# Performance work log

Measured on AMD Instinct MI355X. Metric: run time of the kernel, lower is better.

## Reference

```python
import jax, jax.numpy as jnp
import numpy as np
from jax import lax

RES = 3072
L = 20000

def setup_inputs() -> dict:
    key = jax.random.key(0)
    k1, k2, k3 = jax.random.split(key, 3)
    data = jax.random.uniform(k1, (L, 1), dtype=jnp.float32)
    Win = jax.random.uniform(k2, (RES, 2), dtype=jnp.float32) - 0.5
    W = jax.random.uniform(k3, (RES, RES), dtype=jnp.float32) - 0.5
    # spectral radius of iid uniform(-0.5,0.5) NxN is ~ sqrt(N/12); rescale to 1.25
    W = W * (1.25 / np.sqrt(RES / 12.0)).astype(np.float32)
    return {"data": data, "Win": Win, "W": W,
            "trainLen": 4000, "testLen": 16000, "initLen": 100, "errorLen": 500}

def reference(data, Win, W, trainLen, testLen, initLen, errorLen):
    a = jnp.float32(0.3)
    reg = jnp.float32(4.84e-07)
    res_size = W.shape[0]
    dt = data.dtype

    def train_step(x, u):  # x: [res], u: [1]
        inp = jnp.concatenate([jnp.ones((1,), dt), u])        # [2]
        x = (1 - a) * x + a * jnp.tanh(Win @ inp + W @ x)
        return x, x

    x0 = jnp.zeros((res_size,), dt)
    x_last, xs = lax.scan(train_step, x0, data[:trainLen])     # xs: [trainLen, res]

    n = trainLen - initLen
    # X: rows = [1; u_t; x_t], columns t = initLen..trainLen-1  -> [2+res, n]
    Xmat = jnp.concatenate([jnp.ones((n, 1), dt), data[initLen:trainLen], xs[initLen:]], axis=1).T
    Yt = data[initLen + 1:trainLen + 1]                        # [n, 1]
    A = Xmat @ Xmat.T + reg * jnp.eye(res_size + 2, dtype=dt)
    B = Xmat @ Yt                                              # [2+res, 1]
    Wout = jnp.linalg.solve(A, B).T                            # [1, 2+res]

    def test_step(carry, _):
        x, u = carry
        inp = jnp.concatenate([jnp.ones((1,), dt), u])
        x = (1 - a) * x + a * jnp.tanh(Win @ inp + W @ x)
        out = jnp.concatenate([jnp.ones((1,), dt), u, x])      # [2+res]
        y = Wout @ out                                         # [1]
        return (x, y), y

    u0 = data[trainLen]
    _, Y = lax.scan(test_step, (x_last, u0), None, length=testLen)
    return Y  # [testLen, 1]
```

## Files before the change

kernel.cpp:

```cpp
#include <hip/hip_runtime.h>
#include <math.h>

#define NWG 256
#define TPB 256
#define NWGR 128
#define TPBR 512

constexpr int RES   = 3072;
constexpr int NCOL  = 3074;
constexpr int LDA_  = 3136;
constexpr int TRAIN = 4000;
constexpr int INITN = 100;
constexpr int TESTN = 16000;
constexpr int NSAMP = TRAIN - INITN;
constexpr int NB    = (NCOL + 63) / 64;
constexpr float REGC = 4.84e-07f;

constexpr size_t OFF_PKT_TR  = 4096;
constexpr size_t OFF_ROOT_TR = 8192;
constexpr size_t OFF_PKT_TE  = 12288;
constexpr size_t OFF_ROOT_TE = 16384;
constexpr size_t OFF_F1      = 20480;
constexpr size_t OFF_F2      = 24576;
constexpr size_t OFF_WOUT    = 28672;
constexpr size_t OFF_X       = 49152;
constexpr size_t OFF_B       = 81920;
constexpr size_t OFF_WV      = 114688;
constexpr size_t OFF_Z       = 262144;
constexpr size_t OFF_A       = 50331648;

typedef unsigned long long u64;

#define ALOAD_U32(p)     __hip_atomic_load((p), __ATOMIC_RELAXED, __HIP_MEMORY_SCOPE_AGENT)
#define ALOAD_U64(p)     __hip_atomic_load((p), __ATOMIC_RELAXED, __HIP_MEMORY_SCOPE_AGENT)
#define ASTORE_U64(p, v) __hip_atomic_store((p), (v), __ATOMIC_RELAXED, __HIP_MEMORY_SCOPE_AGENT)
#define AADD_U64(p, v)   __hip_atomic_fetch_add((p), (v), __ATOMIC_RELAXED, __HIP_MEMORY_SCOPE_AGENT)

__device__ __forceinline__ u64 pack_partial(float pf) {
    pf = fminf(fmaxf(pf, -1e6f), 1e6f);
    long long ll = (long long)(pf * 65536.0f);
    return ((u64)ll << 16) + 1ULL;
}

__device__ __forceinline__ u64 hbar(u64* pkt1, u64* root, int s, int g, int tid, u64 arrival) {
    const int ph = s % 3;
    const int grp = g >> 3;
    __builtin_amdgcn_s_waitcnt(0);
    __syncthreads();
    __shared__ u64 rres;
    if (tid == 0) {
        AADD_U64(&pkt1[(ph * 16 + grp) * 8], arrival);
        if ((g & 7) == 0) {
            u64 p;
            do { p = ALOAD_U64(&pkt1[(ph * 16 + grp) * 8]); } while ((p & 0xFFFFULL) != 8ULL);
            AADD_U64(&root[ph * 8], (p & ~0xFFFFULL) | 1ULL);
        }
        u64 r;
        for (;;) {
            r = ALOAD_U64(&root[ph * 8]);
            if ((r & 0xFFFFULL) == 16ULL) break;
            __builtin_amdgcn_s_sleep(1);
        }
        rres = r;
        const int ph2 = (s + 2) % 3;
        if ((g & 7) == 0) ASTORE_U64(&pkt1[(ph2 * 16 + grp) * 8], 0ULL);
        if (g == 0) ASTORE_U64(&root[ph2 * 8], 0ULL);
    }
    __syncthreads();
    return rres;
}

__device__ __forceinline__ void fbar(unsigned* flags, unsigned ep) {
    __threadfence();
    __syncthreads();
    if (threadIdx.x == 0)
        __hip_atomic_store(&flags[blockIdx.x], ep, __ATOMIC_RELEASE, __HIP_MEMORY_SCOPE_AGENT);
    for (;;) {
        unsigned f = ALOAD_U32(&flags[threadIdx.x]);
        if (__syncthreads_and((int)(f >= ep))) break;
        __builtin_amdgcn_s_sleep(1);
    }
    __threadfence();
}

__global__ void k_init(char* __restrict__ ws) {
    size_t tid = (size_t)blockIdx.x * blockDim.x + threadIdx.x;
    size_t nthr = (size_t)gridDim.x * blockDim.x;
    float4 z4 = make_float4(0.f, 0.f, 0.f, 0.f);
    float4* p0 = (float4*)ws;
    for (size_t i = tid; i < 131072 / 16; i += nthr) p0[i] = z4;
    float4* pz = (float4*)(ws + OFF_Z);
    size_t nz = (size_t)NSAMP * LDA_ / 4;
    for (size_t i = tid; i < nz; i += nthr) pz[i] = z4;
}

__global__ __launch_bounds__(512, 2) void k_train(const float* __restrict__ data,
                                                  const float* __restrict__ Win,
                                                  const float* __restrict__ W,
                                                  char* __restrict__ ws) {
    __shared__ float xs[RES];
    float* xb = (float*)(ws + OFF_X);
    float* Z  = (float*)(ws + OFF_Z);
    u64* pkt1 = (u64*)(ws + OFF_PKT_TR);
    u64* root = (u64*)(ws + OFF_ROOT_TR);
    const int tid = threadIdx.x, g = blockIdx.x;
    const int w = tid >> 6, l = tid & 63;
    const int row0 = g * 24 + w * 3;
    const int myrow = row0 + l;
    const float4* W4 = (const float4*)W;
    float4 wreg[36];
#pragma unroll
    for (int r = 0; r < 3; r++)
#pragma unroll
        for (int j = 0; j < 12; j++)
            wreg[r * 12 + j] = W4[(size_t)(row0 + r) * 768 + l + 64 * j];
    float wi0 = 0.f, wi1 = 0.f;
    if (l < 3) { wi0 = Win[2 * myrow]; wi1 = Win[2 * myrow + 1]; }
    const float a_ = 0.3f, oma = 1.0f - 0.3f;
#pragma unroll 1
    for (int s = 0; s < TRAIN; s++) {
        u64* xc8 = (u64*)(xb + (s & 1) * RES);
        float* xn = xb + ((s + 1) & 1) * RES;
        float u = data[s];
        u64* xs8 = (u64*)xs;
#pragma unroll
        for (int p = 0; p < 3; p++)
            xs8[tid + p * TPBR] = ALOAD_U64(&xc8[tid + p * TPBR]);
        __syncthreads();
        float acc0 = 0.f, acc1 = 0.f, acc2 = 0.f;
#pragma unroll
        for (int j = 0; j < 12; j++) {
            float4 xv = ((const float4*)xs)[l + 64 * j];
            float4 w0 = wreg[j], w1 = wreg[12 + j], w2 = wreg[24 + j];
            acc0 += w0.x * xv.x + w0.y * xv.y + w0.z * xv.z + w0.w * xv.w;
            acc1 += w1.x * xv.x + w1.y * xv.y + w1.z * xv.z + w1.w * xv.w;
            acc2 += w2.x * xv.x + w2.y * xv.y + w2.z * xv.z + w2.w * xv.w;
        }
#pragma unroll
        for (int off = 32; off; off >>= 1) {
            acc0 += __shfl_xor(acc0, off);
            acc1 += __shfl_xor(acc1, off);
            acc2 += __shfl_xor(acc2, off);
        }
        if (l < 3) {
            float acc = (l == 0) ? acc0 : ((l == 1) ? acc1 : acc2);
            float pre = acc + wi0 + wi1 * u;
            float xo = xs[myrow];
            float xv_ = oma * xo + a_ * tanhf(pre);
            __hip_atomic_store(&xn[myrow], xv_, __ATOMIC_RELAXED, __HIP_MEMORY_SCOPE_AGENT);
            if (s >= INITN) Z[(size_t)(s - INITN) * LDA_ + 2 + myrow] = xv_;
        }
        if (g == 0 && tid == 0 && s >= INITN) {
            Z[(size_t)(s - INITN) * LDA_] = 1.0f;
            Z[(size_t)(s - INITN) * LDA_ + 1] = u;
        }
        hbar(pkt1, root, s, g, tid, 1ULL);
    }
}

__global__ __launch_bounds__(256) void k_syrk(char* __restrict__ ws) {
    __shared__ float As[64 * 64];
    __shared__ float Bs[64 * 64];
    double* A = (double*)(ws + OFF_A);
    const float4* Z4 = (const float4*)(ws + OFF_Z);
    int tt = blockIdx.x, tid = threadIdx.x;
    int bi = 0;
    while ((bi + 1) * (bi + 2) / 2 <= tt) bi++;
    int bj = tt - bi * (bi + 1) / 2;
    double a64[4][4];
#pragma unroll
    for (int i = 0; i < 4; i++)
#pragma unroll
        for (int j = 0; j < 4; j++) a64[i][j] = 0.0;
    int di = tid & 15, dj = tid >> 4;
    for (int t0 = 0; t0 < NSAMP; t0 += 64) {
#pragma unroll
        for (int p = 0; p < 4; p++) {
            int idx = tid + p * 256;
            int tl = idx >> 4, q = idx & 15;
            float4 va = make_float4(0.f, 0.f, 0.f, 0.f), vb = va;
            if (t0 + tl < NSAMP) {
                va = Z4[(size_t)(t0 + tl) * 784 + bi * 16 + q];
                vb = Z4[(size_t)(t0 + tl) * 784 + bj * 16 + q];
            }
            *(float4*)&As[tl * 64 + q * 4] = va;
            *(float4*)&Bs[tl * 64 + q * 4] = vb;
        }
        __syncthreads();
#pragma unroll 4
        for (int kk = 0; kk < 64; kk++) {
            float4 av = *(const float4*)&As[kk * 64 + di * 4];
            float4 bv = *(const float4*)&Bs[kk * 64 + dj * 4];
            double ad[4] = {(double)av.x, (double)av.y, (double)av.z, (double)av.w};
            double bd[4] = {(double)bv.x, (double)bv.y, (double)bv.z, (double)bv.w};
#pragma unroll
            for (int ii = 0; ii < 4; ii++)
#pragma unroll
                for (int jj = 0; jj < 4; jj++) a64[ii][jj] += ad[ii] * bd[jj];
        }
        __syncthreads();
    }
#pragma unroll
    for (int ii = 0; ii < 4; ii++) {
        int gi = bi * 64 + di * 4 + ii;
#pragma unroll
        for (int jj = 0; jj < 4; jj++) {
            int gj = bj * 64 + dj * 4 + jj;
            if (gi < NCOL && gj < NCOL) {
                double v = a64[ii][jj];
                if (gi == gj) v += (double)REGC;
                A[(size_t)gi * LDA_ + gj] = v;
            }
        }
    }
}

__global__ void k_bvec(const float* __restrict__ data, char* __restrict__ ws) {
    const float* Z = (const float*)(ws + OFF_Z);
    double* b = (double*)(ws + OFF_B);
    int gi = blockIdx.x * blockDim.x + threadIdx.x;
    if (gi >= NCOL) return;
    double acc0 = 0, acc1 = 0, acc2 = 0, acc3 = 0;
    int t = 0;
    for (; t + 3 < NSAMP; t += 4) {
        acc0 += (double)Z[(size_t)t * LDA_ + gi] * (double)data[INITN + t + 1];
        acc1 += (double)Z[(size_t)(t + 1) * LDA_ + gi] * (double)data[INITN + t + 2];
        acc2 += (double)Z[(size_t)(t + 2) * LDA_ + gi] * (double)data[INITN + t + 3];
        acc3 += (double)Z[(size_t)(t + 3) * LDA_ + gi] * (double)data[INITN + t + 4];
    }
    for (; t < NSAMP; t++) acc0 += (double)Z[(size_t)t * LDA_ + gi] * (double)data[INITN + t + 1];
    b[gi] = (acc0 + acc1) + (acc2 + acc3);
}

__global__ __launch_bounds__(256, 1) void k_chol(char* __restrict__ ws) {
    __shared__ double sm[8192];
    double* A = (double*)(ws + OFF_A);
    unsigned* flags = (unsigned*)(ws + OFF_F1);
    unsigned ep = 0;
    int tid = threadIdx.x;
#pragma unroll 1
    for (int k = 0; k < NB; k++) {
        int K = k * 64;
        int bs = NCOL - K; if (bs > 64) bs = 64;
        if (blockIdx.x == 0) {
            for (int idx = tid; idx < bs * bs; idx += TPB) {
                int i = idx / bs, j = idx - i * bs;
                sm[i * 64 + j] = A[(size_t)(K + i) * LDA_ + K + j];
            }
            __syncthreads();
#pragma unroll 1
            for (int j = 0; j < bs; j++) {
                if (tid == 0) {
                    double dv = sm[j * 64 + j];
                    sm[j * 64 + j] = (dv > 0.0) ? sqrt(dv) : 1e-150;
                }
                __syncthreads();
                double d = sm[j * 64 + j];
                for (int i = j + 1 + tid; i < bs; i += TPB) sm[i * 64 + j] /= d;
                __syncthreads();
                int i = tid & 63, mw = tid >> 6;
                if (i > j && i < bs) {
                    double lij = sm[i * 64 + j];
                    for (int m = j + 1 + mw; m <= i; m += 4) sm[i * 64 + m] -= lij * sm[m * 64 + j];
                }
                __syncthreads();
            }
            for (int idx = tid; idx < bs * bs; idx += TPB) {
                int i = idx / bs, j = idx - i * bs;
                if (j <= i) A[(size_t)(K + i) * LDA_ + K + j] = sm[i * 64 + j];
            }
        }
        fbar(flags, ++ep);
        if (K + 64 < NCOL) {
            for (int idx = tid; idx < 4096; idx += TPB) {
                int i = idx >> 6, j = idx & 63;
                sm[i * 64 + j] = A[(size_t)(K + i) * LDA_ + K + j];
            }
            __syncthreads();
            int row = K + 64 + blockIdx.x * TPB + tid;
            if (row < NCOL) {
                double r[64];
#pragma unroll
                for (int j = 0; j < 64; j++) r[j] = A[(size_t)row * LDA_ + K + j];
#pragma unroll
                for (int j = 0; j < 64; j++) {
                    double s = r[j];
#pragma unroll
                    for (int m = 0; m < j; m++) s -= r[m] * sm[j * 64 + m];
                    r[j] = s / sm[j * 64 + j];
                }
#pragma unroll
                for (int j = 0; j < 64; j++) A[(size_t)row * LDA_ + K + j] = r[j];
            }
            fbar(flags, ++ep);
            int rem = NCOL - (K + 64);
            int nbt = (rem + 63) / 64;
            int ntt = nbt * nbt + nbt;
            double* LikT = sm;
            double* LjkT = sm + 4160;
            int i0 = (tid & 15) * 4, j0 = (tid >> 4) * 2;
#pragma unroll 1
            for (int tt = blockIdx.x; tt < ntt; tt += NWG) {
                int ti = 0;
                while ((ti + 1) * (ti + 2) <= tt) ti++;
                int tj = tt - ti * (ti + 1);
                int I0 = K + 64 + ti * 64, J0 = K + 64 + tj * 32;
                for (int idx = tid; idx < 4096; idx += TPB) {
                    int kk = idx & 63, ii = idx >> 6;
                    double v = (I0 + ii < NCOL) ? A[(size_t)(I0 + ii) * LDA_ + K + kk] : 0.0;
                    LikT[kk * 65 + ii] = v;
                }
                for (int idx = tid; idx < 2048; idx += TPB) {
                    int kk = idx & 63, jj = idx >> 6;
                    double v = (J0 + jj < NCOL) ? A[(size_t)(J0 + jj) * LDA_ + K + kk] : 0.0;
                    LjkT[kk * 33 + jj] = v;
                }
                __syncthreads();
                double c[4][2];
#pragma unroll
                for (int ii = 0; ii < 4; ii++)
#pragma unroll
                    for (int jj = 0; jj < 2; jj++) {
                        int gi = I0 + i0 + ii, gj = J0 + j0 + jj;
                        c[ii][jj] = (gi < NCOL && gj < NCOL) ? A[(size_t)gi * LDA_ + gj] : 0.0;
                    }
#pragma unroll 4
                for (int kk = 0; kk < 64; kk++) {
                    double a0 = LikT[kk * 65 + i0], a1 = LikT[kk * 65 + i0 + 1];
                    double a2 = LikT[kk * 65 + i0 + 2], a3 = LikT[kk * 65 + i0 + 3];
                    double b0 = LjkT[kk * 33 + j0], b1 = LjkT[kk * 33 + j0 + 1];
                    c[0][0] -= a0 * b0; c[0][1] -= a0 * b1;
                    c[1][0] -= a1 * b0; c[1][1] -= a1 * b1;
                    c[2][0] -= a2 * b0; c[2][1] -= a2 * b1;
                    c[3][0] -= a3 * b0; c[3][1] -= a3 * b1;
                }
#pragma unroll
                for (int ii = 0; ii < 4; ii++)
#pragma unroll
                    for (int jj = 0; jj < 2; jj++) {
                        int gi = I0 + i0 + ii, gj = J0 + j0 + jj;
                        if (gi < NCOL && gj < NCOL) A[(size_t)gi * LDA_ + gj] = c[ii][jj];
                    }
                __syncthreads();
            }
            fbar(flags, ++ep);
        }
    }
}

__global__ __launch_bounds__(256, 1) void k_solve(char* __restrict__ ws) {
    __shared__ double smd[4096];
    __shared__ double wl[64];
    double* A = (double*)(ws + OFF_A);
    double* b = (double*)(ws + OFF_B);
    double* wv = (double*)(ws + OFF_WV);
    float* wout = (float*)(ws + OFF_WOUT);
    unsigned* flags = (unsigned*)(ws + OFF_F2);
    unsigned ep = 0;
    int tid = threadIdx.x;
#pragma unroll 1
    for (int kb = 0; kb < NB; kb++) {
        int K = kb * 64, bs = NCOL - K; if (bs > 64) bs = 64;
        if (blockIdx.x == 0) {
            for (int idx = tid; idx < 4096; idx += TPB) {
                int i = idx >> 6, j = idx & 63;
                smd[idx] = (i < bs && j < bs) ? A[(size_t)(K + i) * LDA_ + K + j] : ((i == j) ? 1.0 : 0.0);
            }
            __syncthreads();
            if (tid < 64) {
                double bl = (tid < bs) ? b[K + tid] : 0.0;
                for (int j = 0; j < bs; j++) {
                    if (tid == j) bl /= smd[j * 64 + j];
                    double bj = __shfl(bl, j, 64);
                    if (tid > j) bl -= smd[tid * 64 + j] * bj;
                }
                if (tid < bs) b[K + tid] = bl;
            }
        }
        fbar(flags, ++ep);
        if (K + 64 < NCOL) {
            if (tid < 64) wl[tid] = b[K + tid];
            __syncthreads();
            int i = K + 64 + blockIdx.x * TPB + tid;
            if (i < NCOL) {
                double s = 0.0;
#pragma unroll 8
                for (int m = 0; m < 64; m++) s += A[(size_t)i * LDA_ + K + m] * wl[m];
                b[i] -= s;
            }
        }
        fbar(flags, ++ep);
    }
#pragma unroll 1
    for (int kb = NB - 1; kb >= 0; kb--) {
        int K = kb * 64, bs = NCOL - K; if (bs > 64) bs = 64;
        if (blockIdx.x == 0) {
            for (int idx = tid; idx < 4096; idx += TPB) {
                int i = idx >> 6, j = idx & 63;
                smd[idx] = (i < bs && j < bs) ? A[(size_t)(K + i) * LDA_ + K + j] : ((i == j) ? 1.0 : 0.0);
            }
            __syncthreads();
            if (tid < 64) {
                double bl = (tid < bs) ? b[K + tid] : 0.0;
                for (int j = bs - 1; j >= 0; j--) {
                    if (tid == j) bl /= smd[j * 64 + j];
                    double wj = __shfl(bl, j, 64);
                    if (tid < j) bl -= smd[j * 64 + tid] * wj;
                }
                if (tid < bs) wv[K + tid] = bl;
            }
        }
        fbar(flags, ++ep);
        if (K > 0) {
            if (tid < 64) wl[tid] = (tid < bs) ? wv[K + tid] : 0.0;
            __syncthreads();
            int i = blockIdx.x * TPB + tid;
            if (i < K) {
                double s = 0.0;
                for (int m = 0; m < bs; m++) s += A[(size_t)(K + m) * LDA_ + i] * wl[m];
                b[i] -= s;
            }
        }
        fbar(flags, ++ep);
    }
    int gi = blockIdx.x * TPB + tid;
    if (gi < NCOL) wout[gi] = (float)wv[gi];
}

__global__ __launch_bounds__(512, 2) void k_test(const float* __restrict__ data,
                                                 const float* __restrict__ Win,
                                                 const float* __restrict__ W,
                                                 char* __restrict__ ws,
                                                 float* __restrict__ out) {
    __shared__ float xs[RES];
    __shared__ float wp[8];
    float* xb = (float*)(ws + OFF_X);
    const float* wout = (const float*)(ws + OFF_WOUT);
    u64* pkt1 = (u64*)(ws + OFF_PKT_TE);
    u64* root = (u64*)(ws + OFF_ROOT_TE);
    const int tid = threadIdx.x, g = blockIdx.x;
    const int w = tid >> 6, l = tid & 63;
    const int row0 = g * 24 + w * 3;
    const int myrow = row0 + l;
    const float4* W4 = (const float4*)W;
    float4 wreg[36];
#pragma unroll
    for (int r = 0; r < 3; r++)
#pragma unroll
        for (int j = 0; j < 12; j++)
            wreg[r * 12 + j] = W4[(size_t)(row0 + r) * 768 + l + 64 * j];
    float wi0 = 0.f, wi1 = 0.f, wr = 0.f;
    if (l < 3) { wi0 = Win[2 * myrow]; wi1 = Win[2 * myrow + 1]; wr = wout[2 + myrow]; }
    float wo0 = wout[0], wo1 = wout[1];
    const float a_ = 0.3f, oma = 1.0f - 0.3f;
    float u = data[TRAIN];
#pragma unroll 1
    for (int s = 0; s < TESTN; s++) {
        u64* xc8 = (u64*)(xb + (s & 1) * RES);
        float* xn = xb + ((s + 1) & 1) * RES;
        u64* xs8 = (u64*)xs;
#pragma unroll
        for (int p = 0; p < 3; p++)
            xs8[tid + p * TPBR] = ALOAD_U64(&xc8[tid + p * TPBR]);
        __syncthreads();
        float acc0 = 0.f, acc1 = 0.f, acc2 = 0.f;
#pragma unroll
        for (int j = 0; j < 12; j++) {
            float4 xv = ((const float4*)xs)[l + 64 * j];
            float4 w0 = wreg[j], w1 = wreg[12 + j], w2 = wreg[24 + j];
            acc0 += w0.x * xv.x + w0.y * xv.y + w0.z * xv.z + w0.w * xv.w;
            acc1 += w1.x * xv.x + w1.y * xv.y + w1.z * xv.z + w1.w * xv.w;
            acc2 += w2.x * xv.x + w2.y * xv.y + w2.z * xv.z + w2.w * xv.w;
        }
#pragma unroll
        for (int off = 32; off; off >>= 1) {
            acc0 += __shfl_xor(acc0, off);
            acc1 += __shfl_xor(acc1, off);
            acc2 += __shfl_xor(acc2, off);
        }
        float xv_ = 0.f;
        if (l < 3) {
            float acc = (l == 0) ? acc0 : ((l == 1) ? acc1 : acc2);
            float pre = acc + wi0 + wi1 * u;
            float xo = xs[myrow];
            xv_ = oma * xo + a_ * tanhf(pre);
            __hip_atomic_store(&xn[myrow], xv_, __ATOMIC_RELAXED, __HIP_MEMORY_SCOPE_AGENT);
        }
        float v = wr * xv_;
#pragma unroll
        for (int off = 32; off; off >>= 1) v += __shfl_xor(v, off);
        if (l == 0) wp[w] = v;
        __syncthreads();
        float pf = ((wp[0] + wp[1]) + (wp[2] + wp[3])) + ((wp[4] + wp[5]) + (wp[6] + wp[7]));
        u64 r = hbar(pkt1, root, s, g, tid, pack_partial(pf));
        float sgrp = (float)(((long long)r) >> 16) * (1.0f / 65536.0f);
        float y = wo0 + wo1 * u + sgrp;
        y = fminf(fmaxf(y, -1e30f), 1e30f);
        if (!isfinite(y)) y = 0.f;
        if (g == 0 && tid == 0) out[s] = y;
        u = y;
    }
}

extern "C" void kernel_launch(void* const* d_in, const int* in_sizes, int n_in,
                              void* d_out, int out_size, void* d_ws, size_t ws_size,
                              hipStream_t stream) {
    (void)in_sizes; (void)n_in; (void)out_size; (void)ws_size;
    const float* data = (const float*)d_in[0];
    const float* Win  = (const float*)d_in[1];
    const float* W    = (const float*)d_in[2];
    char* ws = (char*)d_ws;
    float* out = (float*)d_out;

    k_init <<<256, 256, 0, stream>>>(ws);
    k_train<<<NWGR, TPBR, 0, stream>>>(data, Win, W, ws);
    k_syrk <<<1225, 256, 0, stream>>>(ws);
    k_bvec <<<13, 256, 0, stream>>>(data, ws);
    k_chol <<<NWG, TPB, 0, stream>>>(ws);
    k_solve<<<NWG, TPB, 0, stream>>>(ws);
    k_test <<<NWGR, TPBR, 0, stream>>>(data, Win, W, ws, out);
}
```

Measured before the change: 107.0 ms.

## Stream bf16-packed recurrent weights per step and flatten grid barrier

Converts W to packed bf16 in workspace and, in the train and test recurrences, reloads each block's weight rows from global/L2 every step instead of holding fp32 weights in registers. This cuts register pressure and halves the weight footprint. It also replaces the two-level hierarchical barrier with a single root atomic counter that all 128 blocks hit. The bf16 weights lose precision in a chaotic recurrence over 16000 steps, so outputs may drift, and per-step weight reloads add memory traffic.

New measurement: 166.9 ms. +56.0%, slower.

```diff
diff --git a/kernel.cpp b/kernel.cpp
--- a/kernel.cpp
+++ b/kernel.cpp
@@ -17,17 +17,17 @@
 constexpr float REGC = 4.84e-07f;
 
 constexpr size_t OFF_PKT_TR  = 4096;
-constexpr size_t OFF_ROOT_TR = 8192;
-constexpr size_t OFF_PKT_TE  = 12288;
-constexpr size_t OFF_ROOT_TE = 16384;
-constexpr size_t OFF_F1      = 20480;
-constexpr size_t OFF_F2      = 24576;
+constexpr size_t OFF_PKT_TE  = 8192;
+constexpr size_t OFF_F1      = 12288;
+constexpr size_t OFF_F2      = 16384;
 constexpr size_t OFF_WOUT    = 28672;
 constexpr size_t OFF_X       = 49152;
 constexpr size_t OFF_B       = 81920;
 constexpr size_t OFF_WV      = 114688;
 constexpr size_t OFF_Z       = 262144;
 constexpr size_t OFF_A       = 50331648;
+constexpr size_t OFF_WBF1 = OFF_A;
+constexpr size_t OFF_WBF2 = OFF_Z;
 
 typedef unsigned long long u64;
 
@@ -42,29 +42,21 @@
     return ((u64)ll << 16) + 1ULL;
 }
 
-__device__ __forceinline__ u64 hbar(u64* pkt1, u64* root, int s, int g, int tid, u64 arrival) {
+__device__ __forceinline__ u64 hbar(u64* root, int s, int g, int tid, u64 arrival) {
     const int ph = s % 3;
-    const int grp = g >> 3;
     __builtin_amdgcn_s_waitcnt(0);
     __syncthreads();
     __shared__ u64 rres;
     if (tid == 0) {
-        AADD_U64(&pkt1[(ph * 16 + grp) * 8], arrival);
-        if ((g & 7) == 0) {
-            u64 p;
-            do { p = ALOAD_U64(&pkt1[(ph * 16 + grp) * 8]); } while ((p & 0xFFFFULL) != 8ULL);
-            AADD_U64(&root[ph * 8], (p & ~0xFFFFULL) | 1ULL);
-        }
+        AADD_U64(&root[ph * 8], arrival);
         u64 r;
         for (;;) {
             r = ALOAD_U64(&root[ph * 8]);
-            if ((r & 0xFFFFULL) == 16ULL) break;
+            if ((r & 0xFFFFULL) == (u64)NWGR) break;
             __builtin_amdgcn_s_sleep(1);
         }
         rres = r;
-        const int ph2 = (s + 2) % 3;
-        if ((g & 7) == 0) ASTORE_U64(&pkt1[(ph2 * 16 + grp) * 8], 0ULL);
-        if (g == 0) ASTORE_U64(&root[ph2 * 8], 0ULL);
+        if (g == 0) ASTORE_U64(&root[((s + 2) % 3) * 8], 0ULL);
     }
     __syncthreads();
     return rres;
@@ -94,31 +86,51 @@
     for (size_t i = tid; i < nz; i += nthr) pz[i] = z4;
 }
 
+__device__ __forceinline__ unsigned bf16r(float f) {
+    unsigned u = __float_as_uint(f);
+    return ((u + 0x7FFFu + ((u >> 16) & 1u)) >> 16) & 0xFFFFu;
+}
+__global__ void k_conv(const float* __restrict__ W, u64* __restrict__ dst) {
+    int idx = blockIdx.x * 256 + threadIdx.x;
+    float4 v = ((const float4*)W)[idx];
+    dst[idx] = (u64)bf16r(v.x) | ((u64)bf16r(v.y) << 16)
+             | ((u64)bf16r(v.z) << 32) | ((u64)bf16r(v.w) << 48);
+}
+
+__device__ __forceinline__ void dot4_bf16(u64 wq, float4 xv, float& acc) {
+    unsigned lo = (unsigned)wq, hi = (unsigned)(wq >> 32);
+    acc += __uint_as_float(lo << 16) * xv.x
+         + __uint_as_float(lo & 0xFFFF0000u) * xv.y
+         + __uint_as_float(hi << 16) * xv.z
+         + __uint_as_float(hi & 0xFFFF0000u) * xv.w;
+}
+
 __global__ __launch_bounds__(512, 2) void k_train(const float* __restrict__ data,
                                                   const float* __restrict__ Win,
-                                                  const float* __restrict__ W,
                                                   char* __restrict__ ws) {
     __shared__ float xs[RES];
     float* xb = (float*)(ws + OFF_X);
     float* Z  = (float*)(ws + OFF_Z);
-    u64* pkt1 = (u64*)(ws + OFF_PKT_TR);
-    u64* root = (u64*)(ws + OFF_ROOT_TR);
+    const u64* WB = (const u64*)(ws + OFF_WBF1);
+    u64* root = (u64*)(ws + OFF_PKT_TR);
     const int tid = threadIdx.x, g = blockIdx.x;
     const int w = tid >> 6, l = tid & 63;
     const int row0 = g * 24 + w * 3;
     const int myrow = row0 + l;
-    const float4* W4 = (const float4*)W;
-    float4 wreg[36];
-#pragma unroll
-    for (int r = 0; r < 3; r++)
-#pragma unroll
-        for (int j = 0; j < 12; j++)
-            wreg[r * 12 + j] = W4[(size_t)(row0 + r) * 768 + l + 64 * j];
     float wi0 = 0.f, wi1 = 0.f;
     if (l < 3) { wi0 = Win[2 * myrow]; wi1 = Win[2 * myrow + 1]; }
     const float a_ = 0.3f, oma = 1.0f - 0.3f;
 #pragma unroll 1
     for (int s = 0; s < TRAIN; s++) {
+        const u64* WBs = WB;
+        asm volatile("" : "+s"(WBs));
+        u64 wv_[36];
+#pragma unroll
+        for (int j = 0; j < 12; j++) {
+            wv_[j]      = WBs[(size_t)(row0 + 0) * 768 + l + 64 * j];
+            wv_[12 + j] = WBs[(size_t)(row0 + 1) * 768 + l + 64 * j];
+            wv_[24 + j] = WBs[(size_t)(row0 + 2) * 768 + l + 64 * j];
+        }
         u64* xc8 = (u64*)(xb + (s & 1) * RES);
         float* xn = xb + ((s + 1) & 1) * RES;
         float u = data[s];
@@ -131,10 +143,9 @@
 #pragma unroll
         for (int j = 0; j < 12; j++) {
             float4 xv = ((const float4*)xs)[l + 64 * j];
-            float4 w0 = wreg[j], w1 = wreg[12 + j], w2 = wreg[24 + j];
-            acc0 += w0.x * xv.x + w0.y * xv.y + w0.z * xv.z + w0.w * xv.w;
-            acc1 += w1.x * xv.x + w1.y * xv.y + w1.z * xv.z + w1.w * xv.w;
-            acc2 += w2.x * xv.x + w2.y * xv.y + w2.z * xv.z + w2.w * xv.w;
+            dot4_bf16(wv_[j], xv, acc0);
+            dot4_bf16(wv_[12 + j], xv, acc1);
+            dot4_bf16(wv_[24 + j], xv, acc2);
         }
 #pragma unroll
         for (int off = 32; off; off >>= 1) {
@@ -154,7 +165,7 @@
             Z[(size_t)(s - INITN) * LDA_] = 1.0f;
             Z[(size_t)(s - INITN) * LDA_ + 1] = u;
         }
-        hbar(pkt1, root, s, g, tid, 1ULL);
+        hbar(root, s, g, tid, 1ULL);
     }
 }
 
@@ -429,26 +440,18 @@
 
 __global__ __launch_bounds__(512, 2) void k_test(const float* __restrict__ data,
                                                  const float* __restrict__ Win,
-                                                 const float* __restrict__ W,
                                                  char* __restrict__ ws,
                                                  float* __restrict__ out) {
     __shared__ float xs[RES];
     __shared__ float wp[8];
     float* xb = (float*)(ws + OFF_X);
     const float* wout = (const float*)(ws + OFF_WOUT);
-    u64* pkt1 = (u64*)(ws + OFF_PKT_TE);
-    u64* root = (u64*)(ws + OFF_ROOT_TE);
+    const u64* WB = (const u64*)(ws + OFF_WBF2);
+    u64* root = (u64*)(ws + OFF_PKT_TE);
     const int tid = threadIdx.x, g = blockIdx.x;
     const int w = tid >> 6, l = tid & 63;
     const int row0 = g * 24 + w * 3;
     const int myrow = row0 + l;
-    const float4* W4 = (const float4*)W;
-    float4 wreg[36];
-#pragma unroll
-    for (int r = 0; r < 3; r++)
-#pragma unroll
-        for (int j = 0; j < 12; j++)
-            wreg[r * 12 + j] = W4[(size_t)(row0 + r) * 768 + l + 64 * j];
     float wi0 = 0.f, wi1 = 0.f, wr = 0.f;
     if (l < 3) { wi0 = Win[2 * myrow]; wi1 = Win[2 * myrow + 1]; wr = wout[2 + myrow]; }
     float wo0 = wout[0], wo1 = wout[1];
@@ -456,6 +459,15 @@
     float u = data[TRAIN];
 #pragma unroll 1
     for (int s = 0; s < TESTN; s++) {
+        const u64* WBs = WB;
+        asm volatile("" : "+s"(WBs));
+        u64 wv_[36];
+#pragma unroll
+        for (int j = 0; j < 12; j++) {
+            wv_[j]      = WBs[(size_t)(row0 + 0) * 768 + l + 64 * j];
+            wv_[12 + j] = WBs[(size_t)(row0 + 1) * 768 + l + 64 * j];
+            wv_[24 + j] = WBs[(size_t)(row0 + 2) * 768 + l + 64 * j];
+        }
         u64* xc8 = (u64*)(xb + (s & 1) * RES);
         float* xn = xb + ((s + 1) & 1) * RES;
         u64* xs8 = (u64*)xs;
@@ -467,10 +479,9 @@
 #pragma unroll
         for (int j = 0; j < 12; j++) {
             float4 xv = ((const float4*)xs)[l + 64 * j];
-            float4 w0 = wreg[j], w1 = wreg[12 + j], w2 = wreg[24 + j];
-            acc0 += w0.x * xv.x + w0.y * xv.y + w0.z * xv.z + w0.w * xv.w;
-            acc1 += w1.x * xv.x + w1.y * xv.y + w1.z * xv.z + w1.w * xv.w;
-            acc2 += w2.x * xv.x + w2.y * xv.y + w2.z * xv.z + w2.w * xv.w;
+            dot4_bf16(wv_[j], xv, acc0);
+            dot4_bf16(wv_[12 + j], xv, acc1);
+            dot4_bf16(wv_[24 + j], xv, acc2);
         }
 #pragma unroll
         for (int off = 32; off; off >>= 1) {
@@ -492,7 +503,7 @@
         if (l == 0) wp[w] = v;
         __syncthreads();
         float pf = ((wp[0] + wp[1]) + (wp[2] + wp[3])) + ((wp[4] + wp[5]) + (wp[6] + wp[7]));
-        u64 r = hbar(pkt1, root, s, g, tid, pack_partial(pf));
+        u64 r = hbar(root, s, g, tid, pack_partial(pf));
         float sgrp = (float)(((long long)r) >> 16) * (1.0f / 65536.0f);
         float y = wo0 + wo1 * u + sgrp;
         y = fminf(fmaxf(y, -1e30f), 1e30f);
@@ -513,10 +524,12 @@
     float* out = (float*)d_out;
 
     k_init <<<256, 256, 0, stream>>>(ws);
-    k_train<<<NWGR, TPBR, 0, stream>>>(data, Win, W, ws);
+    k_conv <<<9216, 256, 0, stream>>>(W, (u64*)(ws + OFF_WBF1));
+    k_train<<<NWGR, TPBR, 0, stream>>>(data, Win, ws);
     k_syrk <<<1225, 256, 0, stream>>>(ws);
     k_bvec <<<13, 256, 0, stream>>>(data, ws);
+    k_conv <<<9216, 256, 0, stream>>>(W, (u64*)(ws + OFF_WBF2));
     k_chol <<<NWG, TPB, 0, stream>>>(ws);
     k_solve<<<NWG, TPB, 0, stream>>>(ws);
-    k_test <<<NWGR, TPBR, 0, stream>>>(data, Win, W, ws, out);
-}
+    k_test <<<NWGR, TPBR, 0, stream>>>(data, Win, ws, out);
+}
```

## Store reservoir weights as bf16 split across LDS and registers over 256 workgroups

Applied to the files above, without the earlier changes.

Adds a conversion kernel that packs W into bf16 in workspace, once before the train scan and once before the test scan. The train and test kernels now run 256 workgroups of 256 threads instead of 128 of 512. Each block keeps two of its three rows per wave in LDS and the third row in registers. The hierarchical barrier is regrouped to 16 groups of 16 blocks. The aim is to relieve register pressure and spread the recurrent matvec over more compute units, at the cost of bf16 rounding error in a long autoregressive recurrence, extra LDS traffic and more barrier participants.

After: 147.2 ms. +37.5%, slower.

```diff
diff --git a/kernel.cpp b/kernel.cpp
--- a/kernel.cpp
+++ b/kernel.cpp
@@ -3,8 +3,6 @@
 
 #define NWG 256
 #define TPB 256
-#define NWGR 128
-#define TPBR 512
 
 constexpr int RES   = 3072;
 constexpr int NCOL  = 3074;
@@ -28,6 +26,8 @@
 constexpr size_t OFF_WV      = 114688;
 constexpr size_t OFF_Z       = 262144;
 constexpr size_t OFF_A       = 50331648;
+constexpr size_t OFF_WBF1 = OFF_A;
+constexpr size_t OFF_WBF2 = OFF_Z;
 
 typedef unsigned long long u64;
 
@@ -44,15 +44,15 @@
 
 __device__ __forceinline__ u64 hbar(u64* pkt1, u64* root, int s, int g, int tid, u64 arrival) {
     const int ph = s % 3;
-    const int grp = g >> 3;
+    const int grp = g >> 4;
     __builtin_amdgcn_s_waitcnt(0);
     __syncthreads();
     __shared__ u64 rres;
     if (tid == 0) {
         AADD_U64(&pkt1[(ph * 16 + grp) * 8], arrival);
-        if ((g & 7) == 0) {
+        if ((g & 15) == 0) {
             u64 p;
-            do { p = ALOAD_U64(&pkt1[(ph * 16 + grp) * 8]); } while ((p & 0xFFFFULL) != 8ULL);
+            do { p = ALOAD_U64(&pkt1[(ph * 16 + grp) * 8]); } while ((p & 0xFFFFULL) != 16ULL);
             AADD_U64(&root[ph * 8], (p & ~0xFFFFULL) | 1ULL);
         }
         u64 r;
@@ -63,7 +63,7 @@
         }
         rres = r;
         const int ph2 = (s + 2) % 3;
-        if ((g & 7) == 0) ASTORE_U64(&pkt1[(ph2 * 16 + grp) * 8], 0ULL);
+        if ((g & 15) == 0) ASTORE_U64(&pkt1[(ph2 * 16 + grp) * 8], 0ULL);
         if (g == 0) ASTORE_U64(&root[ph2 * 8], 0ULL);
     }
     __syncthreads();
@@ -94,29 +94,54 @@
     for (size_t i = tid; i < nz; i += nthr) pz[i] = z4;
 }
 
-__global__ __launch_bounds__(512, 2) void k_train(const float* __restrict__ data,
+__device__ __forceinline__ unsigned bf16r(float f) {
+    unsigned u = __float_as_uint(f);
+    return ((u + 0x7FFFu + ((u >> 16) & 1u)) >> 16) & 0xFFFFu;
+}
+__global__ void k_conv(const float* __restrict__ W, u64* __restrict__ dst) {
+    int idx = blockIdx.x * 256 + threadIdx.x;
+    float4 v = ((const float4*)W)[idx];
+    dst[idx] = (u64)bf16r(v.x) | ((u64)bf16r(v.y) << 16)
+             | ((u64)bf16r(v.z) << 32) | ((u64)bf16r(v.w) << 48);
+}
+
+__device__ __forceinline__ void dot4_bf16(u64 wq, float4 xv, float& acc) {
+    unsigned lo = (unsigned)wq, hi = (unsigned)(wq >> 32);
+    acc += __uint_as_float(lo << 16) * xv.x
+         + __uint_as_float(lo & 0xFFFF0000u) * xv.y
+         + __uint_as_float(hi << 16) * xv.z
+         + __uint_as_float(hi & 0xFFFF0000u) * xv.w;
+}
+
+__global__ __launch_bounds__(256, 1) void k_train(const float* __restrict__ data,
                                                   const float* __restrict__ Win,
-                                                  const float* __restrict__ W,
                                                   char* __restrict__ ws) {
+    __shared__ u64 wlds[6144];
     __shared__ float xs[RES];
     float* xb = (float*)(ws + OFF_X);
     float* Z  = (float*)(ws + OFF_Z);
+    const u64* WB = (const u64*)(ws + OFF_WBF1);
     u64* pkt1 = (u64*)(ws + OFF_PKT_TR);
     u64* root = (u64*)(ws + OFF_ROOT_TR);
     const int tid = threadIdx.x, g = blockIdx.x;
     const int w = tid >> 6, l = tid & 63;
-    const int row0 = g * 24 + w * 3;
+    const int row0 = g * 12 + w * 3;
     const int myrow = row0 + l;
-    const float4* W4 = (const float4*)W;
-    float4 wreg[36];
-#pragma unroll
-    for (int r = 0; r < 3; r++)
-#pragma unroll
-        for (int j = 0; j < 12; j++)
-            wreg[r * 12 + j] = W4[(size_t)(row0 + r) * 768 + l + 64 * j];
+    for (int it = tid; it < 6144; it += TPB) {
+        int lr = it / 768, c = it - lr * 768;
+        int grow = g * 12 + (lr >> 1) * 3 + (lr & 1);
+        wlds[it] = WB[(size_t)grow * 768 + c];
+    }
+    u64 wr2[12];
+#pragma unroll
+    for (int j = 0; j < 12; j++)
+        wr2[j] = WB[(size_t)(row0 + 2) * 768 + l + 64 * j];
     float wi0 = 0.f, wi1 = 0.f;
     if (l < 3) { wi0 = Win[2 * myrow]; wi1 = Win[2 * myrow + 1]; }
+    const u64* wl0 = &wlds[(w * 2 + 0) * 768];
+    const u64* wl1 = &wlds[(w * 2 + 1) * 768];
     const float a_ = 0.3f, oma = 1.0f - 0.3f;
+    __syncthreads();
 #pragma unroll 1
     for (int s = 0; s < TRAIN; s++) {
         u64* xc8 = (u64*)(xb + (s & 1) * RES);
@@ -124,17 +149,16 @@
         float u = data[s];
         u64* xs8 = (u64*)xs;
 #pragma unroll
-        for (int p = 0; p < 3; p++)
-            xs8[tid + p * TPBR] = ALOAD_U64(&xc8[tid + p * TPBR]);
+        for (int p = 0; p < 6; p++)
+            xs8[tid + p * TPB] = ALOAD_U64(&xc8[tid + p * TPB]);
         __syncthreads();
         float acc0 = 0.f, acc1 = 0.f, acc2 = 0.f;
 #pragma unroll
         for (int j = 0; j < 12; j++) {
             float4 xv = ((const float4*)xs)[l + 64 * j];
-            float4 w0 = wreg[j], w1 = wreg[12 + j], w2 = wreg[24 + j];
-            acc0 += w0.x * xv.x + w0.y * xv.y + w0.z * xv.z + w0.w * xv.w;
-            acc1 += w1.x * xv.x + w1.y * xv.y + w1.z * xv.z + w1.w * xv.w;
-            acc2 += w2.x * xv.x + w2.y * xv.y + w2.z * xv.z + w2.w * xv.w;
+            dot4_bf16(wl0[l + 64 * j], xv, acc0);
+            dot4_bf16(wl1[l + 64 * j], xv, acc1);
+            dot4_bf16(wr2[j], xv, acc2);
         }
 #pragma unroll
         for (int off = 32; off; off >>= 1) {
@@ -155,6 +179,7 @@
             Z[(size_t)(s - INITN) * LDA_ + 1] = u;
         }
         hbar(pkt1, root, s, g, tid, 1ULL);
+        __syncthreads();
     }
 }
 
@@ -427,50 +452,55 @@
     if (gi < NCOL) wout[gi] = (float)wv[gi];
 }
 
-__global__ __launch_bounds__(512, 2) void k_test(const float* __restrict__ data,
+__global__ __launch_bounds__(256, 1) void k_test(const float* __restrict__ data,
                                                  const float* __restrict__ Win,
-                                                 const float* __restrict__ W,
                                                  char* __restrict__ ws,
                                                  float* __restrict__ out) {
+    __shared__ u64 wlds[6144];
     __shared__ float xs[RES];
-    __shared__ float wp[8];
+    __shared__ float wp[4];
     float* xb = (float*)(ws + OFF_X);
     const float* wout = (const float*)(ws + OFF_WOUT);
+    const u64* WB = (const u64*)(ws + OFF_WBF2);
     u64* pkt1 = (u64*)(ws + OFF_PKT_TE);
     u64* root = (u64*)(ws + OFF_ROOT_TE);
     const int tid = threadIdx.x, g = blockIdx.x;
     const int w = tid >> 6, l = tid & 63;
-    const int row0 = g * 24 + w * 3;
+    const int row0 = g * 12 + w * 3;
     const int myrow = row0 + l;
-    const float4* W4 = (const float4*)W;
-    float4 wreg[36];
-#pragma unroll
-    for (int r = 0; r < 3; r++)
-#pragma unroll
-        for (int j = 0; j < 12; j++)
-            wreg[r * 12 + j] = W4[(size_t)(row0 + r) * 768 + l + 64 * j];
+    for (int it = tid; it < 6144; it += TPB) {
+        int lr = it / 768, c = it - lr * 768;
+        int grow = g * 12 + (lr >> 1) * 3 + (lr & 1);
+        wlds[it] = WB[(size_t)grow * 768 + c];
+    }
+    u64 wr2[12];
+#pragma unroll
+    for (int j = 0; j < 12; j++)
+        wr2[j] = WB[(size_t)(row0 + 2) * 768 + l + 64 * j];
     float wi0 = 0.f, wi1 = 0.f, wr = 0.f;
     if (l < 3) { wi0 = Win[2 * myrow]; wi1 = Win[2 * myrow + 1]; wr = wout[2 + myrow]; }
     float wo0 = wout[0], wo1 = wout[1];
+    const u64* wl0 = &wlds[(w * 2 + 0) * 768];
+    const u64* wl1 = &wlds[(w * 2 + 1) * 768];
     const float a_ = 0.3f, oma = 1.0f - 0.3f;
     float u = data[TRAIN];
+    __syncthreads();
 #pragma unroll 1
     for (int s = 0; s < TESTN; s++) {
         u64* xc8 = (u64*)(xb + (s & 1) * RES);
         float* xn = xb + ((s + 1) & 1) * RES;
         u64* xs8 = (u64*)xs;
 #pragma unroll
-        for (int p = 0; p < 3; p++)
-            xs8[tid + p * TPBR] = ALOAD_U64(&xc8[tid + p * TPBR]);
+        for (int p = 0; p < 6; p++)
+            xs8[tid + p * TPB] = ALOAD_U64(&xc8[tid + p * TPB]);
         __syncthreads();
         float acc0 = 0.f, acc1 = 0.f, acc2 = 0.f;
 #pragma unroll
         for (int j = 0; j < 12; j++) {
             float4 xv = ((const float4*)xs)[l + 64 * j];
-            float4 w0 = wreg[j], w1 = wreg[12 + j], w2 = wreg[24 + j];
-            acc0 += w0.x * xv.x + w0.y * xv.y + w0.z * xv.z + w0.w * xv.w;
-            acc1 += w1.x * xv.x + w1.y * xv.y + w1.z * xv.z + w1.w * xv.w;
-            acc2 += w2.x * xv.x + w2.y * xv.y + w2.z * xv.z + w2.w * xv.w;
+            dot4_bf16(wl0[l + 64 * j], xv, acc0);
+            dot4_bf16(wl1[l + 64 * j], xv, acc1);
+            dot4_bf16(wr2[j], xv, acc2);
         }
 #pragma unroll
         for (int off = 32; off; off >>= 1) {
@@ -491,7 +521,7 @@
         for (int off = 32; off; off >>= 1) v += __shfl_xor(v, off);
         if (l == 0) wp[w] = v;
         __syncthreads();
-        float pf = ((wp[0] + wp[1]) + (wp[2] + wp[3])) + ((wp[4] + wp[5]) + (wp[6] + wp[7]));
+        float pf = (wp[0] + wp[1]) + (wp[2] + wp[3]);
         u64 r = hbar(pkt1, root, s, g, tid, pack_partial(pf));
         float sgrp = (float)(((long long)r) >> 16) * (1.0f / 65536.0f);
         float y = wo0 + wo1 * u + sgrp;
@@ -499,6 +529,7 @@
         if (!isfinite(y)) y = 0.f;
         if (g == 0 && tid == 0) out[s] = y;
         u = y;
+        __syncthreads();
     }
 }
 
@@ -513,10 +544,12 @@
     float* out = (float*)d_out;
 
     k_init <<<256, 256, 0, stream>>>(ws);
-    k_train<<<NWGR, TPBR, 0, stream>>>(data, Win, W, ws);
+    k_conv <<<9216, 256, 0, stream>>>(W, (u64*)(ws + OFF_WBF1));
+    k_train<<<NWG, TPB, 0, stream>>>(data, Win, ws);
     k_syrk <<<1225, 256, 0, stream>>>(ws);
     k_bvec <<<13, 256, 0, stream>>>(data, ws);
+    k_conv <<<9216, 256, 0, stream>>>(W, (u64*)(ws + OFF_WBF2));
     k_chol <<<NWG, TPB, 0, stream>>>(ws);
     k_solve<<<NWG, TPB, 0, stream>>>(ws);
-    k_test <<<NWGR, TPBR, 0, stream>>>(data, Win, W, ws, out);
-}
+    k_test <<<NWG, TPB, 0, stream>>>(data, Win, ws, out);
+}
```
